# Optimization experiments

Measured on AMD Instinct MI355X. Metric: run time of the kernel, lower is better.

Reference implementation:

```python
import jax, jax.numpy as jnp
import numpy as np

D_MODEL = 512
D_STATE = 16
EXPAND = 2
DT_RANK = 8
D_INNER = EXPAND * D_MODEL  # 1024
LN_EPS = 1e-5


def setup_inputs() -> dict:
    key = jax.random.key(0)
    ks = jax.random.split(key, 10)
    B, H, W = 8, 48, 48
    inp = {
        "x": jax.random.normal(ks[0], (B, H, W, D_MODEL), jnp.float32),
        # Linear weights stored [in, out] (torch weight transposed)
        "W_in": jax.random.normal(ks[1], (D_MODEL, 2 * D_INNER), jnp.float32) * 0.02,
        # depthwise conv kernel, HWIO with feature_group_count = D_INNER
        "conv_k": jax.random.normal(ks[2], (3, 3, 1, D_INNER), jnp.float32) * 0.1,
        "W_xproj": jax.random.normal(ks[3], (D_INNER, DT_RANK + 2 * D_STATE), jnp.float32) * 0.02,
        "W_dt": jax.random.uniform(ks[4], (DT_RANK, D_INNER), jnp.float32, -0.1, 0.1),
        "b_dt": jnp.full((D_INNER,), 0.1, jnp.float32),
        "A_log": jax.random.normal(ks[5], (D_STATE,), jnp.float32) * 0.02,
        "Dskip": jnp.ones((D_INNER,), jnp.float32),
        "W_dtN": jax.random.normal(ks[6], (D_INNER, D_STATE), jnp.float32) * 0.02,
        "b_dtN": jnp.zeros((D_STATE,), jnp.float32),
        "ln_g": jnp.ones((D_INNER,), jnp.float32),
        "ln_b": jnp.zeros((D_INNER,), jnp.float32),
        "W_out": jax.random.normal(ks[7], (D_INNER, D_MODEL), jnp.float32) * 0.02,
        "b_out": jnp.zeros((D_MODEL,), jnp.float32),
    }
    return inp


def _ss2d(x, W_in, conv_k, W_xproj, W_dt, b_dt, A_log, Dskip, W_dtN, b_dtN,
          ln_g, ln_b, W_out, b_out):
    B, H, W_, _ = x.shape
    L = H * W_
    # in_proj and split into x / gate z
    xz = x @ W_in                                   # [B,H,W,2*D_INNER]
    xh, z = jnp.split(xz, 2, axis=-1)
    # depthwise 3x3 conv (NHWC)
    xc = jax.lax.conv_general_dilated(
        xh, conv_k, window_strides=(1, 1), padding='SAME',
        dimension_numbers=('NHWC', 'HWIO', 'NHWC'),
        feature_group_count=D_INNER)                 # [B,H,W,D_INNER]
    # x_proj -> (dt_rank, B, C)
    xp = xc @ W_xproj
    dt_r = xp[..., :DT_RANK]
    Bp = xp[..., DT_RANK:DT_RANK + D_STATE]
    Cp = xp[..., DT_RANK + D_STATE:]
    dt = dt_r @ W_dt + b_dt                          # [B,H,W,D_INNER]
    # flatten spatial dims into sequence
    x_seq = xc.reshape(B, L, D_INNER)
    dt_seq = jax.nn.softplus(dt.reshape(B, L, D_INNER))
    B_seq = Bp.reshape(B, L, D_STATE)
    C_seq = Cp.reshape(B, L, D_STATE)
    A = -jnp.exp(A_log)                              # [N]; A_log expanded over D is constant per-row
    dtN = dt_seq @ W_dtN + b_dtN                     # dt_to_N_proj(softplus(dt)) -> [B,L,N]

    def step(h, t):
        x_t, dt_t, dtN_t, B_t, C_t = t               # [B,D],[B,D],[B,N],[B,N],[B,N]
        dA = jnp.exp(dt_t[:, :, None] * A)           # [B,D,N]
        dB = dtN_t * B_t                             # [B,N]
        h = dA * h + dB[:, None, :] * x_t[:, :, None]  # [B,D,N]
        y = jnp.einsum('bdn,bn->bd', h, C_t) + Dskip * x_t
        return h, y

    h0 = jnp.zeros((B, D_INNER, D_STATE), x.dtype)
    xs = (x_seq.transpose(1, 0, 2), dt_seq.transpose(1, 0, 2),
          dtN.transpose(1, 0, 2), B_seq.transpose(1, 0, 2),
          C_seq.transpose(1, 0, 2))
    _, ys = jax.lax.scan(step, h0, xs)               # ys: [L,B,D]
    y = ys.transpose(1, 0, 2).reshape(B, H, W_, D_INNER)
    # LayerNorm over channel dim
    mu = y.mean(-1, keepdims=True)
    var = ((y - mu) ** 2).mean(-1, keepdims=True)
    y = (y - mu) / jnp.sqrt(var + LN_EPS) * ln_g + ln_b
    # gate and out projection (dropout = identity in eval)
    y = y * jax.nn.silu(z)
    return y @ W_out + b_out


def reference(x, W_in, conv_k, W_xproj, W_dt, b_dt, A_log, Dskip, W_dtN,
              b_dtN, ln_g, ln_b, W_out, b_out):
    return _ss2d(x, W_in, conv_k, W_xproj, W_dt, b_dt, A_log, Dskip, W_dtN,
                 b_dtN, ln_g, ln_b, W_out, b_out)
```

## Files before the change

### kernel.cpp

```cpp
#include <hip/hip_runtime.h>
#include <hip/hip_bf16.h>

#define NBATCH 8
#define HEIGHT 48
#define WIDTH  48
#define DMODEL 512
#define DSTATE 16
#define DTRANK 8
#define DINNER 1024
#define LSEQ   (HEIGHT*WIDTH)
#define NROWS  (NBATCH*LSEQ)
#define NXP    40
#define NCH    64
#define TCH    36

typedef unsigned short u16;
typedef unsigned int   u32;
typedef __attribute__((ext_vector_type(8))) short short8;
typedef __attribute__((ext_vector_type(4))) float f32x4;

__device__ __forceinline__ float bf2f(u16 u) {
    u32 x = ((u32)u) << 16;
    return __uint_as_float(x);
}
__device__ __forceinline__ u16 f2bf(float f) {
    u32 x = __float_as_uint(f);
    u32 r = (x + 0x7FFFu + ((x >> 16) & 1u)) >> 16;
    return (u16)r;
}

#if __has_builtin(__builtin_amdgcn_exp2f)
__device__ __forceinline__ float EXP2(float x) { return __builtin_amdgcn_exp2f(x); }
#else
__device__ __forceinline__ float EXP2(float x) { return __expf(x * 0.69314718f); }
#endif

#define GLD16(g, l) __builtin_amdgcn_global_load_lds( \
    (const __attribute__((address_space(1))) void*)(g), \
    (__attribute__((address_space(3))) void*)(l), 16, 0, 0)

__global__ __launch_bounds__(256) void k_prep_x(const float* __restrict__ x,
                                                u16* __restrict__ xbf) {
    int i = blockIdx.x * 256 + threadIdx.x;
    float4 v = *reinterpret_cast<const float4*>(x + (size_t)i * 4);
    ushort4 o;
    o.x = f2bf(v.x); o.y = f2bf(v.y); o.z = f2bf(v.z); o.w = f2bf(v.w);
    *reinterpret_cast<ushort4*>(xbf + (size_t)i * 4) = o;
}

__global__ __launch_bounds__(256) void k_prep_w(const float* __restrict__ W_in,
                                                const float* __restrict__ W_out,
                                                const float* __restrict__ W_xproj,
                                                const float* __restrict__ W_dtN,
                                                u16* __restrict__ WinT,
                                                u16* __restrict__ WoutT,
                                                u16* __restrict__ WxpB,
                                                u16* __restrict__ WdtNB) {
    int idx = blockIdx.x * 256 + threadIdx.x;
    if (idx < 2048 * 512) {
        int n = idx >> 9, k = idx & 511;
        WinT[idx] = f2bf(W_in[(size_t)k * 2048 + n]);
    } else if (idx < 2048 * 512 + 512 * 1024) {
        int j = idx - 2048 * 512;
        int n = j >> 10, k = j & 1023;
        WoutT[j] = f2bf(W_out[(size_t)k * 512 + n]);
    } else if (idx < 2048 * 512 + 512 * 1024 + 48 * 1024) {
        int j = idx - (2048 * 512 + 512 * 1024);
        int n = j >> 10, k = j & 1023;
        WxpB[j] = (n < NXP) ? f2bf(W_xproj[(size_t)k * NXP + n]) : (u16)0;
    } else {
        int j = idx - (2048 * 512 + 512 * 1024 + 48 * 1024);
        int n = j >> 10, k = j & 1023;
        WdtNB[j] = f2bf(W_dtN[(size_t)k * DSTATE + n]);
    }
}

template<int K, int LDA, int LDB, int LDC, bool F32OUT>
__global__ __launch_bounds__(256) void k_gemm_mfma(const u16* __restrict__ A,
                                                   const u16* __restrict__ B,
                                                   const float* __restrict__ bias,
                                                   void* __restrict__ Cv) {
    __shared__ u16 As[128 * 32];
    __shared__ u16 Bs[128 * 32];
    const int tid = threadIdx.x;
    const int l   = tid & 63;
    const int w   = tid >> 6;
    const int wm  = w >> 1, wn = w & 1;
    const int id   = blockIdx.y * gridDim.x + blockIdx.x;
    const int nwg  = gridDim.x * gridDim.y;
    const int swz  = (id & 7) * (nwg >> 3) + (id >> 3);
    const int bx   = swz % gridDim.x;
    const int by   = swz / gridDim.x;
    const int m0  = by * 128, n0 = bx * 128;
    const int srow = w * 32 + (l >> 2);
    const int sc   = l & 3;
    const int kh = l >> 4;
    const int lr = l & 15;

    f32x4 acc[4][4];
#pragma unroll
    for (int i = 0; i < 4; ++i)
#pragma unroll
        for (int j = 0; j < 4; ++j)
            acc[i][j] = (f32x4){0.f, 0.f, 0.f, 0.f};

    for (int k0 = 0; k0 < K; k0 += 32) {
#pragma unroll
        for (int i = 0; i < 2; ++i) {
            int r  = srow + i * 16;
            int cg = sc ^ ((r >> 1) & 3);
            const u16* ga = A + (size_t)(m0 + r) * LDA + k0 + cg * 8;
            const u16* gb = B + (size_t)(n0 + r) * LDB + k0 + cg * 8;
            GLD16(ga, As + (w * 2 + i) * 512);
            GLD16(gb, Bs + (w * 2 + i) * 512);
        }
        __syncthreads();
        short8 af[4], bfr[4];
#pragma unroll
        for (int f = 0; f < 4; ++f) {
            int ar = wm * 64 + f * 16 + lr;
            af[f]  = *reinterpret_cast<const short8*>(As + ar * 32 + ((kh ^ ((ar >> 1) & 3)) * 8));
            int br = wn * 64 + f * 16 + lr;
            bfr[f] = *reinterpret_cast<const short8*>(Bs + br * 32 + ((kh ^ ((br >> 1) & 3)) * 8));
        }
#pragma unroll
        for (int fm = 0; fm < 4; ++fm)
#pragma unroll
            for (int fn = 0; fn < 4; ++fn)
                acc[fm][fn] = __builtin_amdgcn_mfma_f32_16x16x32_bf16(
                    af[fm], bfr[fn], acc[fm][fn], 0, 0, 0);
        __syncthreads();
    }

#pragma unroll
    for (int fm = 0; fm < 4; ++fm) {
#pragma unroll
        for (int r = 0; r < 4; ++r) {
            int row = m0 + wm * 64 + fm * 16 + (l >> 4) * 4 + r;
#pragma unroll
            for (int fn = 0; fn < 4; ++fn) {
                int col = n0 + wn * 64 + fn * 16 + lr;
                if (F32OUT) {
                    ((float*)Cv)[(size_t)row * LDC + col] = acc[fm][fn][r] + bias[col];
                } else {
                    ((u16*)Cv)[(size_t)row * LDC + col] = f2bf(acc[fm][fn][r]);
                }
            }
        }
    }
}

__global__ __launch_bounds__(256) void k_conv(const u16* __restrict__ xz,
                                              const float* __restrict__ ck,
                                              u16* __restrict__ xc) {
    const int blk = blockIdx.x;
    const int wg = blk % (WIDTH / 8);
    const int hb = blk / (WIDTH / 8);
    const int h = hb % HEIGHT;
    const int b = hb / HEIGHT;
    const int w0 = wg * 8;
    const int c0 = threadIdx.x * 4;

    float acc[8][4];
#pragma unroll
    for (int j = 0; j < 8; ++j)
#pragma unroll
        for (int q = 0; q < 4; ++q) acc[j][q] = 0.f;

#pragma unroll
    for (int kh = 0; kh < 3; ++kh) {
        int hh = h + kh - 1;
        if (hh < 0 || hh >= HEIGHT) continue;
        const u16* rp = xz + ((size_t)(b * HEIGHT + hh) * WIDTH) * 2048 + c0;
        float a[10][4];
#pragma unroll
        for (int i = 0; i < 10; ++i) {
            int ww = w0 - 1 + i;
            if (ww >= 0 && ww < WIDTH) {
                ushort4 v = *reinterpret_cast<const ushort4*>(rp + (size_t)ww * 2048);
                a[i][0] = bf2f(v.x); a[i][1] = bf2f(v.y);
                a[i][2] = bf2f(v.z); a[i][3] = bf2f(v.w);
            } else {
                a[i][0] = a[i][1] = a[i][2] = a[i][3] = 0.f;
            }
        }
#pragma unroll
        for (int kw = 0; kw < 3; ++kw) {
            float4 kv = *reinterpret_cast<const float4*>(ck + (kh * 3 + kw) * DINNER + c0);
#pragma unroll
            for (int j = 0; j < 8; ++j) {
                acc[j][0] = fmaf(a[j + kw][0], kv.x, acc[j][0]);
                acc[j][1] = fmaf(a[j + kw][1], kv.y, acc[j][1]);
                acc[j][2] = fmaf(a[j + kw][2], kv.z, acc[j][2]);
                acc[j][3] = fmaf(a[j + kw][3], kv.w, acc[j][3]);
            }
        }
    }
    const size_t orow = (size_t)((b * HEIGHT + h) * WIDTH + w0);
#pragma unroll
    for (int j = 0; j < 8; ++j) {
        ushort4 ov;
        ov.x = f2bf(acc[j][0]); ov.y = f2bf(acc[j][1]);
        ov.z = f2bf(acc[j][2]); ov.w = f2bf(acc[j][3]);
        *reinterpret_cast<ushort4*>(xc + (orow + j) * DINNER + c0) = ov;
    }
}

__global__ __launch_bounds__(256) void k_xproj(const u16* __restrict__ xc,
                                               const u16* __restrict__ WxpB,
                                               float* __restrict__ xp_out) {
    __shared__ u16 As[64 * 32];
    __shared__ u16 Bs[48 * 32];
    const int tid = threadIdx.x;
    const int l = tid & 63;
    const int w = tid >> 6;
    const int m0 = blockIdx.x * 64;
    const int kh = l >> 4, lr = l & 15;
    const int srow = w * 16 + (l >> 2);
    const int sc = l & 3;

    f32x4 acc[3];
    acc[0] = acc[1] = acc[2] = (f32x4){0.f, 0.f, 0.f, 0.f};

    for (int k0 = 0; k0 < 1024; k0 += 32) {
        {
            int cg = sc ^ ((srow >> 1) & 3);
            GLD16(xc + (size_t)(m0 + srow) * DINNER + k0 + cg * 8, As + w * 512);
            if (w < 3)
                GLD16(WxpB + (size_t)srow * 1024 + k0 + cg * 8, Bs + w * 512);
        }
        __syncthreads();
        int ar = w * 16 + lr;
        short8 af = *reinterpret_cast<const short8*>(As + ar * 32 + ((kh ^ ((ar >> 1) & 3)) * 8));
#pragma unroll
        for (int fn = 0; fn < 3; ++fn) {
            int br = fn * 16 + lr;
            short8 bf = *reinterpret_cast<const short8*>(Bs + br * 32 + ((kh ^ ((br >> 1) & 3)) * 8));
            acc[fn] = __builtin_amdgcn_mfma_f32_16x16x32_bf16(af, bf, acc[fn], 0, 0, 0);
        }
        __syncthreads();
    }
#pragma unroll
    for (int fn = 0; fn < 3; ++fn)
#pragma unroll
        for (int r = 0; r < 4; ++r) {
            int row = m0 + w * 16 + (l >> 4) * 4 + r;
            int col = fn * 16 + lr;
            if (col < NXP) xp_out[(size_t)row * NXP + col] = acc[fn][r];
        }
}

__global__ __launch_bounds__(256) void k_dt(const float* __restrict__ xp,
                                            const float* __restrict__ W_dt,
                                            const float* __restrict__ b_dt,
                                            u16* __restrict__ dt_out) {
    int gid = blockIdx.x * 256 + threadIdx.x;
    int row = gid >> 7;
    int dj  = (gid & 127) * 8;
    const float* xr = xp + (size_t)row * NXP;
    float4 xa = *reinterpret_cast<const float4*>(xr);
    float4 xb = *reinterpret_cast<const float4*>(xr + 4);
    float xv[8] = {xa.x, xa.y, xa.z, xa.w, xb.x, xb.y, xb.z, xb.w};
    float a[8];
    {
        float4 b0 = *reinterpret_cast<const float4*>(b_dt + dj);
        float4 b1 = *reinterpret_cast<const float4*>(b_dt + dj + 4);
        a[0]=b0.x; a[1]=b0.y; a[2]=b0.z; a[3]=b0.w;
        a[4]=b1.x; a[5]=b1.y; a[6]=b1.z; a[7]=b1.w;
    }
#pragma unroll
    for (int j = 0; j < 8; ++j) {
        float4 w0 = *reinterpret_cast<const float4*>(W_dt + j * DINNER + dj);
        float4 w1 = *reinterpret_cast<const float4*>(W_dt + j * DINNER + dj + 4);
        a[0] = fmaf(xv[j], w0.x, a[0]); a[1] = fmaf(xv[j], w0.y, a[1]);
        a[2] = fmaf(xv[j], w0.z, a[2]); a[3] = fmaf(xv[j], w0.w, a[3]);
        a[4] = fmaf(xv[j], w1.x, a[4]); a[5] = fmaf(xv[j], w1.y, a[5]);
        a[6] = fmaf(xv[j], w1.z, a[6]); a[7] = fmaf(xv[j], w1.w, a[7]);
    }
    short8 o;
#pragma unroll
    for (int j = 0; j < 8; ++j) {
        float dt = fmaxf(a[j], 0.f) + log1pf(__expf(-fabsf(a[j])));
        o[j] = (short)f2bf(dt);
    }
    *reinterpret_cast<short8*>(dt_out + (size_t)row * DINNER + dj) = o;
}

__global__ __launch_bounds__(256) void k_dtn(const u16* __restrict__ dtb,
                                             const u16* __restrict__ WdtNB,
                                             const float* __restrict__ b_dtN,
                                             const float* __restrict__ xp,
                                             float* __restrict__ dnBC) {
    __shared__ u16 As[64 * 32];
    __shared__ u16 Bs[16 * 32];
    const int tid = threadIdx.x;
    const int l = tid & 63;
    const int w = tid >> 6;
    const int m0 = blockIdx.x * 64;
    const int kh = l >> 4, lr = l & 15;
    const int srow = w * 16 + (l >> 2);
    const int sc = l & 3;

    f32x4 acc = (f32x4){0.f, 0.f, 0.f, 0.f};

    for (int k0 = 0; k0 < 1024; k0 += 32) {
        {
            int cg = sc ^ ((srow >> 1) & 3);
            GLD16(dtb + (size_t)(m0 + srow) * DINNER + k0 + cg * 8, As + w * 512);
            if (w == 0)
                GLD16(WdtNB + (size_t)srow * 1024 + k0 + cg * 8, Bs);
        }
        __syncthreads();
        int ar = w * 16 + lr;
        short8 af = *reinterpret_cast<const short8*>(As + ar * 32 + ((kh ^ ((ar >> 1) & 3)) * 8));
        short8 bf = *reinterpret_cast<const short8*>(Bs + lr * 32 + ((kh ^ ((lr >> 1) & 3)) * 8));
        acc = __builtin_amdgcn_mfma_f32_16x16x32_bf16(af, bf, acc, 0, 0, 0);
        __syncthreads();
    }
    float bn = b_dtN[lr];
#pragma unroll
    for (int r = 0; r < 4; ++r) {
        int row = m0 + w * 16 + (l >> 4) * 4 + r;
        float dn = acc[r] + bn;
        float Bv = xp[(size_t)row * NXP + DTRANK + lr];
        float Cv = xp[(size_t)row * NXP + DTRANK + DSTATE + lr];
        dnBC[(size_t)row * 32 + lr]      = dn * Bv;
        dnBC[(size_t)row * 32 + 16 + lr] = Cv;
    }
}

#define P1_N(IDX, COMP) \
    dA = EXP2(dt * An2[IDX]); h[IDX] = fmaf(dA, h[IDX], COMP * xt);

#define P1_BODY(T, DTC, XCC, DTN, XCN, PR) { \
    const float4* sv = pS + (size_t)(T) * 8; \
    float4 u0 = sv[0], u1 = sv[1], u2 = sv[2], u3 = sv[3]; \
    if (PR) { DTN = pdt[(size_t)((T) + 1) * DINNER]; \
              XCN = pxc[(size_t)((T) + 1) * DINNER]; } \
    float dt = bf2f(DTC), xt = bf2f(XCC); \
    sdt += dt; \
    float dA; \
    P1_N(0,  u0.x) P1_N(1,  u0.y) P1_N(2,  u0.z) P1_N(3,  u0.w) \
    P1_N(4,  u1.x) P1_N(5,  u1.y) P1_N(6,  u1.z) P1_N(7,  u1.w) \
    P1_N(8,  u2.x) P1_N(9,  u2.y) P1_N(10, u2.z) P1_N(11, u2.w) \
    P1_N(12, u3.x) P1_N(13, u3.y) P1_N(14, u3.z) P1_N(15, u3.w) }

__global__ __launch_bounds__(256) void k_scan_p1(const u16* __restrict__ xc,
                                                 const u16* __restrict__ dtb,
                                                 const float* __restrict__ dnBC,
                                                 const float* __restrict__ A_log,
                                                 float* __restrict__ sdt_out,
                                                 float* __restrict__ Qbuf) {
    const int tid = threadIdx.x;
    const int id  = blockIdx.x;
    const int swz = (id & 7) * ((NBATCH * NCH * 4) >> 3) + (id >> 3);
    const int quarter = swz & 3;
    const int bc = swz >> 2;
    const int c = bc & (NCH - 1);
    const int b = bc >> 6;
    const int d = quarter * 256 + tid;

    float An2[16];
#pragma unroll
    for (int n = 0; n < 16; ++n)
        An2[n] = -__expf(A_log[n]) * 1.44269504f;

    float h[16];
#pragma unroll
    for (int n = 0; n < 16; ++n) h[n] = 0.f;
    float sdt = 0.f;

    const size_t row0 = (size_t)b * LSEQ + (size_t)c * TCH;
    const u16* pdt = dtb + row0 * DINNER + d;
    const u16* pxc = xc  + row0 * DINNER + d;
    const float4* pS = reinterpret_cast<const float4*>(dnBC + row0 * 32);

    u16 dtA = pdt[0], xcA = pxc[0];
    u16 dtB, xcB;

    for (int t = 0; t < TCH - 2; t += 2) {
        P1_BODY(t,     dtA, xcA, dtB, xcB, true)
        P1_BODY(t + 1, dtB, xcB, dtA, xcA, true)
    }
    P1_BODY(TCH - 2, dtA, xcA, dtB, xcB, true)
    P1_BODY(TCH - 1, dtB, xcB, dtA, xcA, false)

    sdt_out[(size_t)bc * DINNER + d] = sdt;
    size_t base = ((size_t)bc << 14) + d;
#pragma unroll
    for (int n = 0; n < 16; ++n)
        Qbuf[base + (size_t)n * DINNER] = h[n];
}

__global__ __launch_bounds__(256) void k_scan_p2(const float* __restrict__ sdt,
                                                 const float* __restrict__ A_log,
                                                 float* __restrict__ Qbuf) {
    int tid = blockIdx.x * 256 + threadIdx.x;
    int b = tid >> 14, rem = tid & 16383;
    int n = rem >> 10, d = rem & 1023;
    float An2 = -__expf(A_log[n]) * 1.44269504f;
    float h = 0.f;
    for (int c = 0; c < NCH; ++c) {
        int bc = b * NCH + c;
        float P = EXP2(sdt[(size_t)bc * DINNER + d] * An2);
        size_t idx = ((size_t)bc << 14) + rem;
        float q = Qbuf[idx];
        Qbuf[idx] = h;
        h = fmaf(P, h, q);
    }
}

#define P3_N(IDX, UC, CC, YS) \
    dA = EXP2(dt * An2[IDX]); h[IDX] = fmaf(dA, h[IDX], UC * xt); \
    YS = fmaf(h[IDX], CC, YS);

#define P3_BODY(T, DTC, XCC, DTN, XCN, PR) { \
    const float4* sv = pS + (size_t)(T) * 8; \
    float4 u0 = sv[0], u1 = sv[1], u2 = sv[2], u3 = sv[3]; \
    float4 c4 = sv[4], c5 = sv[5], c6 = sv[6], c7 = sv[7]; \
    if (PR) { DTN = pdt[(size_t)((T) + 1) * DINNER]; \
              XCN = pxc[(size_t)((T) + 1) * DINNER]; } \
    float dt = bf2f(DTC), xt = bf2f(XCC); \
    float ys0 = Dsk * xt, ys1 = 0.f, ys2 = 0.f, ys3 = 0.f; \
    float dA; \
    P3_N(0,  u0.x, c4.x, ys0) P3_N(1,  u0.y, c4.y, ys1) \
    P3_N(2,  u0.z, c4.z, ys2) P3_N(3,  u0.w, c4.w, ys3) \
    P3_N(4,  u1.x, c5.x, ys0) P3_N(5,  u1.y, c5.y, ys1) \
    P3_N(6,  u1.z, c5.z, ys2) P3_N(7,  u1.w, c5.w, ys3) \
    P3_N(8,  u2.x, c6.x, ys0) P3_N(9,  u2.y, c6.y, ys1) \
    P3_N(10, u2.z, c6.z, ys2) P3_N(11, u2.w, c6.w, ys3) \
    P3_N(12, u3.x, c7.x, ys0) P3_N(13, u3.y, c7.y, ys1) \
    P3_N(14, u3.z, c7.z, ys2) P3_N(15, u3.w, c7.w, ys3) \
    ybuf[(row0 + (T)) * 2048 + d] = f2bf((ys0 + ys1) + (ys2 + ys3)); }

__global__ __launch_bounds__(256) void k_scan_p3(const u16* __restrict__ xc,
                                                 const u16* __restrict__ dtb,
                                                 const float* __restrict__ dnBC,
                                                 const float* __restrict__ A_log,
                                                 const float* __restrict__ Dskip,
                                                 const float* __restrict__ Qbuf,
                                                 u16* __restrict__ ybuf) {
    const int tid = threadIdx.x;
    const int id  = blockIdx.x;
    const int swz = (id & 7) * ((NBATCH * NCH * 4) >> 3) + (id >> 3);
    const int quarter = swz & 3;
    const int bc = swz >> 2;
    const int c = bc & (NCH - 1);
    const int b = bc >> 6;
    const int d = quarter * 256 + tid;

    float An2[16];
#pragma unroll
    for (int n = 0; n < 16; ++n)
        An2[n] = -__expf(A_log[n]) * 1.44269504f;

    float h[16];
    size_t base = ((size_t)bc << 14) + d;
#pragma unroll
    for (int n = 0; n < 16; ++n) h[n] = Qbuf[base + (size_t)n * DINNER];
    float Dsk = Dskip[d];

    const size_t row0 = (size_t)b * LSEQ + (size_t)c * TCH;
    const u16* pdt = dtb + row0 * DINNER + d;
    const u16* pxc = xc  + row0 * DINNER + d;
    const float4* pS = reinterpret_cast<const float4*>(dnBC + row0 * 32);

    u16 dtA = pdt[0], xcA = pxc[0];
    u16 dtB, xcB;

    for (int t = 0; t < TCH - 2; t += 2) {
        P3_BODY(t,     dtA, xcA, dtB, xcB, true)
        P3_BODY(t + 1, dtB, xcB, dtA, xcA, true)
    }
    P3_BODY(TCH - 2, dtA, xcA, dtB, xcB, true)
    P3_BODY(TCH - 1, dtB, xcB, dtA, xcA, false)
}

__global__ __launch_bounds__(256) void k_ln_gate(u16* __restrict__ xz,
                                                 const float* __restrict__ ln_g,
                                                 const float* __restrict__ ln_b) {
    __shared__ float red[8];
    int row = blockIdx.x, tid = threadIdx.x;
    u16* yrow = xz + (size_t)row * 2048;
    int c0 = tid * 4;
    ushort4 v = *reinterpret_cast<const ushort4*>(yrow + c0);
    float y0 = bf2f(v.x), y1 = bf2f(v.y), y2 = bf2f(v.z), y3 = bf2f(v.w);
    float s = y0 + y1 + y2 + y3;
    float q = y0 * y0 + y1 * y1 + y2 * y2 + y3 * y3;
#pragma unroll
    for (int m = 32; m; m >>= 1) {
        s += __shfl_xor(s, m, 64);
        q += __shfl_xor(q, m, 64);
    }
    int lane = tid & 63, wv = tid >> 6;
    if (lane == 0) { red[wv] = s; red[4 + wv] = q; }
    __syncthreads();
    s = red[0] + red[1] + red[2] + red[3];
    q = red[4] + red[5] + red[6] + red[7];
    float mu = s * (1.f / DINNER);
    float var = q * (1.f / DINNER) - mu * mu;
    float rstd = rsqrtf(var + 1e-5f);
    ushort4 zv = *reinterpret_cast<const ushort4*>(yrow + DINNER + c0);
    float4 lg = *reinterpret_cast<const float4*>(ln_g + c0);
    float4 lb = *reinterpret_cast<const float4*>(ln_b + c0);
    float z0 = bf2f(zv.x), z1 = bf2f(zv.y), z2 = bf2f(zv.z), z3 = bf2f(zv.w);
    float g0 = ((y0 - mu) * rstd * lg.x + lb.x) * (z0 / (1.f + __expf(-z0)));
    float g1 = ((y1 - mu) * rstd * lg.y + lb.y) * (z1 / (1.f + __expf(-z1)));
    float g2 = ((y2 - mu) * rstd * lg.z + lb.z) * (z2 / (1.f + __expf(-z2)));
    float g3 = ((y3 - mu) * rstd * lg.w + lb.w) * (z3 / (1.f + __expf(-z3)));
    ushort4 ov;
    ov.x = f2bf(g0); ov.y = f2bf(g1); ov.z = f2bf(g2); ov.w = f2bf(g3);
    *reinterpret_cast<ushort4*>(yrow + c0) = ov;
}

extern "C" void kernel_launch(void* const* d_in, const int* in_sizes, int n_in,
                              void* d_out, int out_size, void* d_ws, size_t ws_size,
                              hipStream_t stream) {
    const float* x       = (const float*)d_in[0];
    const float* W_in    = (const float*)d_in[1];
    const float* conv_k  = (const float*)d_in[2];
    const float* W_xproj = (const float*)d_in[3];
    const float* W_dt    = (const float*)d_in[4];
    const float* b_dt    = (const float*)d_in[5];
    const float* A_log   = (const float*)d_in[6];
    const float* Dskip   = (const float*)d_in[7];
    const float* W_dtN   = (const float*)d_in[8];
    const float* b_dtN   = (const float*)d_in[9];
    const float* ln_g    = (const float*)d_in[10];
    const float* ln_b    = (const float*)d_in[11];
    const float* W_out   = (const float*)d_in[12];
    const float* b_out   = (const float*)d_in[13];
    float* out = (float*)d_out;

    char* ws = (char*)d_ws;
    size_t off = 0;
    u16*   xz    = (u16*)(ws + off); off += (size_t)NROWS * 2048 * 2;
    u16*   xc    = (u16*)(ws + off); off += (size_t)NROWS * 1024 * 2;
    u16*   dtb   = (u16*)(ws + off); off += (size_t)NROWS * 1024 * 2;
    float* xpb   = (float*)(ws + off); off += (size_t)NROWS * NXP * 4;
    float* dnBC  = (float*)(ws + off); off += (size_t)NROWS * 32 * 4;
    char*  scr   = ws + off; off += (size_t)NBATCH * NCH * DINNER * DSTATE * 4;
    u16*   xbf   = (u16*)scr;
    float* Qbuf  = (float*)scr;
    float* sdtb  = xpb;
    u16*   WinT  = (u16*)(ws + off); off += (size_t)2048 * 512 * 2;
    u16*   WoutT = (u16*)(ws + off); off += (size_t)512 * 1024 * 2;
    u16*   WxpB  = (u16*)(ws + off); off += (size_t)48 * 1024 * 2;
    u16*   WdtNB = (u16*)(ws + off); off += (size_t)16 * 1024 * 2;

    k_prep_x<<<(NROWS * DMODEL / 4) / 256, 256, 0, stream>>>(x, xbf);
    k_prep_w<<<(2048 * 512 + 512 * 1024 + 48 * 1024 + 16 * 1024) / 256, 256, 0, stream>>>(
        W_in, W_out, W_xproj, W_dtN, WinT, WoutT, WxpB, WdtNB);
    k_gemm_mfma<512, 512, 512, 2048, false>
        <<<dim3(2048 / 128, NROWS / 128), 256, 0, stream>>>(xbf, WinT, nullptr, xz);
    k_conv<<<NBATCH * HEIGHT * (WIDTH / 8), 256, 0, stream>>>(xz, conv_k, xc);
    k_xproj<<<NROWS / 64, 256, 0, stream>>>(xc, WxpB, xpb);
    k_dt<<<(NROWS * DINNER / 8) / 256, 256, 0, stream>>>(xpb, W_dt, b_dt, dtb);
    k_dtn<<<NROWS / 64, 256, 0, stream>>>(dtb, WdtNB, b_dtN, xpb, dnBC);
    k_scan_p1<<<NBATCH * NCH * 4, 256, 0, stream>>>(xc, dtb, dnBC, A_log,
                                                    sdtb, Qbuf);
    k_scan_p2<<<(NBATCH * DINNER * DSTATE) / 256, 256, 0, stream>>>(sdtb, A_log, Qbuf);
    k_scan_p3<<<NBATCH * NCH * 4, 256, 0, stream>>>(xc, dtb, dnBC, A_log,
                                                    Dskip, Qbuf, xz);
    k_ln_gate<<<NROWS, 256, 0, stream>>>(xz, ln_g, ln_b);
    k_gemm_mfma<1024, 2048, 1024, 512, true>
        <<<dim3(DMODEL / 128, NROWS / 128), 256, 0, stream>>>(xz, WoutT, b_out, out);
}
```

Before: 330.9 us.

## Fuse x_proj with dt projection, split-K skinny GEMMs, merge prep kernels

Merges the x and weight bf16 prep kernels into one launch, and fuses the x_proj GEMM with the dt low-rank projection plus softplus so xp does not need a round trip for dt. The skinny x_proj and dt_N GEMMs are restructured as 16-row tiles with split-K across four waves, reading operands straight from global memory and reducing through LDS instead of staging through LDS with barriers. It also raises wave priority around the scan inner math. The aim is fewer launches, more blocks for these narrow GEMMs and less barrier overhead. The cost is an extra LDS reduction and redundant W_dt loads per block.

```diff
diff --git a/kernel.cpp b/kernel.cpp
--- a/kernel.cpp
+++ b/kernel.cpp
@@ -39,24 +39,25 @@
     (const __attribute__((address_space(1))) void*)(g), \
     (__attribute__((address_space(3))) void*)(l), 16, 0, 0)
 
-__global__ __launch_bounds__(256) void k_prep_x(const float* __restrict__ x,
-                                                u16* __restrict__ xbf) {
-    int i = blockIdx.x * 256 + threadIdx.x;
-    float4 v = *reinterpret_cast<const float4*>(x + (size_t)i * 4);
-    ushort4 o;
-    o.x = f2bf(v.x); o.y = f2bf(v.y); o.z = f2bf(v.z); o.w = f2bf(v.w);
-    *reinterpret_cast<ushort4*>(xbf + (size_t)i * 4) = o;
-}
-
-__global__ __launch_bounds__(256) void k_prep_w(const float* __restrict__ W_in,
-                                                const float* __restrict__ W_out,
-                                                const float* __restrict__ W_xproj,
-                                                const float* __restrict__ W_dtN,
-                                                u16* __restrict__ WinT,
-                                                u16* __restrict__ WoutT,
-                                                u16* __restrict__ WxpB,
-                                                u16* __restrict__ WdtNB) {
-    int idx = blockIdx.x * 256 + threadIdx.x;
+__global__ __launch_bounds__(256) void k_prep(const float* __restrict__ x,
+                                              const float* __restrict__ W_in,
+                                              const float* __restrict__ W_out,
+                                              const float* __restrict__ W_xproj,
+                                              const float* __restrict__ W_dtN,
+                                              u16* __restrict__ xbf,
+                                              u16* __restrict__ WinT,
+                                              u16* __restrict__ WoutT,
+                                              u16* __restrict__ WxpB,
+                                              u16* __restrict__ WdtNB) {
+    if (blockIdx.x < 9216) {
+        int i = blockIdx.x * 256 + threadIdx.x;
+        float4 v = *reinterpret_cast<const float4*>(x + (size_t)i * 4);
+        ushort4 o;
+        o.x = f2bf(v.x); o.y = f2bf(v.y); o.z = f2bf(v.z); o.w = f2bf(v.w);
+        *reinterpret_cast<ushort4*>(xbf + (size_t)i * 4) = o;
+        return;
+    }
+    int idx = (blockIdx.x - 9216) * 256 + threadIdx.x;
     if (idx < 2048 * 512) {
         int n = idx >> 9, k = idx & 511;
         WinT[idx] = f2bf(W_in[(size_t)k * 2048 + n]);
@@ -206,84 +207,71 @@
     }
 }
 
-__global__ __launch_bounds__(256) void k_xproj(const u16* __restrict__ xc,
-                                               const u16* __restrict__ WxpB,
-                                               float* __restrict__ xp_out) {
-    __shared__ u16 As[64 * 32];
-    __shared__ u16 Bs[48 * 32];
+__global__ __launch_bounds__(256) void k_xproj_dt(const u16* __restrict__ xc,
+                                                  const u16* __restrict__ WxpB,
+                                                  const float* __restrict__ W_dt,
+                                                  const float* __restrict__ b_dt,
+                                                  float* __restrict__ xp_out,
+                                                  u16* __restrict__ dt_out) {
+    __shared__ float R[4][16][48];
+    __shared__ float xpS[16][8];
     const int tid = threadIdx.x;
-    const int l = tid & 63;
-    const int w = tid >> 6;
-    const int m0 = blockIdx.x * 64;
-    const int kh = l >> 4, lr = l & 15;
-    const int srow = w * 16 + (l >> 2);
-    const int sc = l & 3;
+    const int l = tid & 63, w = tid >> 6;
+    const int m0 = blockIdx.x * 16;
+    const int lr = l & 15, kh = l >> 4;
+    const int kbase = w * 256;
 
     f32x4 acc[3];
     acc[0] = acc[1] = acc[2] = (f32x4){0.f, 0.f, 0.f, 0.f};
-
-    for (int k0 = 0; k0 < 1024; k0 += 32) {
-        {
-            int cg = sc ^ ((srow >> 1) & 3);
-            GLD16(xc + (size_t)(m0 + srow) * DINNER + k0 + cg * 8, As + w * 512);
-            if (w < 3)
-                GLD16(WxpB + (size_t)srow * 1024 + k0 + cg * 8, Bs + w * 512);
-        }
-        __syncthreads();
-        int ar = w * 16 + lr;
-        short8 af = *reinterpret_cast<const short8*>(As + ar * 32 + ((kh ^ ((ar >> 1) & 3)) * 8));
+    const u16* arow = xc + (size_t)(m0 + lr) * DINNER + kbase + kh * 8;
+#pragma unroll
+    for (int ks = 0; ks < 256; ks += 32) {
+        short8 af = *reinterpret_cast<const short8*>(arow + ks);
 #pragma unroll
         for (int fn = 0; fn < 3; ++fn) {
-            int br = fn * 16 + lr;
-            short8 bf = *reinterpret_cast<const short8*>(Bs + br * 32 + ((kh ^ ((br >> 1) & 3)) * 8));
+            short8 bf = *reinterpret_cast<const short8*>(
+                WxpB + (size_t)(fn * 16 + lr) * DINNER + kbase + ks + kh * 8);
             acc[fn] = __builtin_amdgcn_mfma_f32_16x16x32_bf16(af, bf, acc[fn], 0, 0, 0);
         }
-        __syncthreads();
     }
 #pragma unroll
     for (int fn = 0; fn < 3; ++fn)
 #pragma unroll
-        for (int r = 0; r < 4; ++r) {
-            int row = m0 + w * 16 + (l >> 4) * 4 + r;
-            int col = fn * 16 + lr;
-            if (col < NXP) xp_out[(size_t)row * NXP + col] = acc[fn][r];
-        }
-}
-
-__global__ __launch_bounds__(256) void k_dt(const float* __restrict__ xp,
-                                            const float* __restrict__ W_dt,
-                                            const float* __restrict__ b_dt,
-                                            u16* __restrict__ dt_out) {
-    int gid = blockIdx.x * 256 + threadIdx.x;
-    int row = gid >> 7;
-    int dj  = (gid & 127) * 8;
-    const float* xr = xp + (size_t)row * NXP;
-    float4 xa = *reinterpret_cast<const float4*>(xr);
-    float4 xb = *reinterpret_cast<const float4*>(xr + 4);
-    float xv[8] = {xa.x, xa.y, xa.z, xa.w, xb.x, xb.y, xb.z, xb.w};
-    float a[8];
-    {
-        float4 b0 = *reinterpret_cast<const float4*>(b_dt + dj);
-        float4 b1 = *reinterpret_cast<const float4*>(b_dt + dj + 4);
-        a[0]=b0.x; a[1]=b0.y; a[2]=b0.z; a[3]=b0.w;
-        a[4]=b1.x; a[5]=b1.y; a[6]=b1.z; a[7]=b1.w;
-    }
+        for (int r = 0; r < 4; ++r)
+            R[w][(l >> 4) * 4 + r][fn * 16 + lr] = acc[fn][r];
+    __syncthreads();
+    for (int i = tid; i < 16 * 48; i += 256) {
+        int row = i / 48, col = i % 48;
+        float s = R[0][row][col] + R[1][row][col] + R[2][row][col] + R[3][row][col];
+        if (col < NXP) xp_out[(size_t)(m0 + row) * NXP + col] = s;
+        if (col < 8) xpS[row][col] = s;
+    }
+    __syncthreads();
+    const int d4 = tid * 4;
+    float wreg[8][4];
 #pragma unroll
     for (int j = 0; j < 8; ++j) {
-        float4 w0 = *reinterpret_cast<const float4*>(W_dt + j * DINNER + dj);
-        float4 w1 = *reinterpret_cast<const float4*>(W_dt + j * DINNER + dj + 4);
-        a[0] = fmaf(xv[j], w0.x, a[0]); a[1] = fmaf(xv[j], w0.y, a[1]);
-        a[2] = fmaf(xv[j], w0.z, a[2]); a[3] = fmaf(xv[j], w0.w, a[3]);
-        a[4] = fmaf(xv[j], w1.x, a[4]); a[5] = fmaf(xv[j], w1.y, a[5]);
-        a[6] = fmaf(xv[j], w1.z, a[6]); a[7] = fmaf(xv[j], w1.w, a[7]);
-    }
-    short8 o;
-#pragma unroll
-    for (int j = 0; j < 8; ++j) {
-        float dt = fmaxf(a[j], 0.f) + log1pf(__expf(-fabsf(a[j])));
-        o[j] = (short)f2bf(dt);
-    }
-    *reinterpret_cast<short8*>(dt_out + (size_t)row * DINNER + dj) = o;
+        float4 wv = *reinterpret_cast<const float4*>(W_dt + j * DINNER + d4);
+        wreg[j][0] = wv.x; wreg[j][1] = wv.y; wreg[j][2] = wv.z; wreg[j][3] = wv.w;
+    }
+    float4 bb = *reinterpret_cast<const float4*>(b_dt + d4);
+    for (int row = 0; row < 16; ++row) {
+        float a0 = bb.x, a1 = bb.y, a2 = bb.z, a3 = bb.w;
+#pragma unroll
+        for (int j = 0; j < 8; ++j) {
+            float xj = xpS[row][j];
+            a0 = fmaf(xj, wreg[j][0], a0);
+            a1 = fmaf(xj, wreg[j][1], a1);
+            a2 = fmaf(xj, wreg[j][2], a2);
+            a3 = fmaf(xj, wreg[j][3], a3);
+        }
+        ushort4 o;
+        o.x = f2bf(fmaxf(a0, 0.f) + log1pf(__expf(-fabsf(a0))));
+        o.y = f2bf(fmaxf(a1, 0.f) + log1pf(__expf(-fabsf(a1))));
+        o.z = f2bf(fmaxf(a2, 0.f) + log1pf(__expf(-fabsf(a2))));
+        o.w = f2bf(fmaxf(a3, 0.f) + log1pf(__expf(-fabsf(a3))));
+        *reinterpret_cast<ushort4*>(dt_out + (size_t)(m0 + row) * DINNER + d4) = o;
+    }
 }
 
 __global__ __launch_bounds__(256) void k_dtn(const u16* __restrict__ dtb,
@@ -291,42 +279,32 @@
                                              const float* __restrict__ b_dtN,
                                              const float* __restrict__ xp,
                                              float* __restrict__ dnBC) {
-    __shared__ u16 As[64 * 32];
-    __shared__ u16 Bs[16 * 32];
+    __shared__ float R[4][16][16];
     const int tid = threadIdx.x;
-    const int l = tid & 63;
-    const int w = tid >> 6;
-    const int m0 = blockIdx.x * 64;
-    const int kh = l >> 4, lr = l & 15;
-    const int srow = w * 16 + (l >> 2);
-    const int sc = l & 3;
+    const int l = tid & 63, w = tid >> 6;
+    const int m0 = blockIdx.x * 16;
+    const int lr = l & 15, kh = l >> 4;
+    const int kbase = w * 256;
 
     f32x4 acc = (f32x4){0.f, 0.f, 0.f, 0.f};
-
-    for (int k0 = 0; k0 < 1024; k0 += 32) {
-        {
-            int cg = sc ^ ((srow >> 1) & 3);
-            GLD16(dtb + (size_t)(m0 + srow) * DINNER + k0 + cg * 8, As + w * 512);
-            if (w == 0)
-                GLD16(WdtNB + (size_t)srow * 1024 + k0 + cg * 8, Bs);
-        }
-        __syncthreads();
-        int ar = w * 16 + lr;
-        short8 af = *reinterpret_cast<const short8*>(As + ar * 32 + ((kh ^ ((ar >> 1) & 3)) * 8));
-        short8 bf = *reinterpret_cast<const short8*>(Bs + lr * 32 + ((kh ^ ((lr >> 1) & 3)) * 8));
+    const u16* arow = dtb + (size_t)(m0 + lr) * DINNER + kbase + kh * 8;
+    const u16* brow = WdtNB + (size_t)lr * DINNER + kbase + kh * 8;
+#pragma unroll
+    for (int ks = 0; ks < 256; ks += 32) {
+        short8 af = *reinterpret_cast<const short8*>(arow + ks);
+        short8 bf = *reinterpret_cast<const short8*>(brow + ks);
         acc = __builtin_amdgcn_mfma_f32_16x16x32_bf16(af, bf, acc, 0, 0, 0);
-        __syncthreads();
-    }
-    float bn = b_dtN[lr];
-#pragma unroll
-    for (int r = 0; r < 4; ++r) {
-        int row = m0 + w * 16 + (l >> 4) * 4 + r;
-        float dn = acc[r] + bn;
-        float Bv = xp[(size_t)row * NXP + DTRANK + lr];
-        float Cv = xp[(size_t)row * NXP + DTRANK + DSTATE + lr];
-        dnBC[(size_t)row * 32 + lr]      = dn * Bv;
-        dnBC[(size_t)row * 32 + 16 + lr] = Cv;
-    }
+    }
+#pragma unroll
+    for (int r = 0; r < 4; ++r)
+        R[w][(l >> 4) * 4 + r][lr] = acc[r];
+    __syncthreads();
+    int row = tid >> 4, n = tid & 15;
+    float dn = R[0][row][n] + R[1][row][n] + R[2][row][n] + R[3][row][n] + b_dtN[n];
+    float Bv = xp[(size_t)(m0 + row) * NXP + DTRANK + n];
+    float Cv = xp[(size_t)(m0 + row) * NXP + DTRANK + DSTATE + n];
+    dnBC[(size_t)(m0 + row) * 32 + n]      = dn * Bv;
+    dnBC[(size_t)(m0 + row) * 32 + 16 + n] = Cv;
 }
 
 #define P1_N(IDX, COMP) \
@@ -340,10 +318,12 @@
     float dt = bf2f(DTC), xt = bf2f(XCC); \
     sdt += dt; \
     float dA; \
+    __builtin_amdgcn_s_setprio(1); \
     P1_N(0,  u0.x) P1_N(1,  u0.y) P1_N(2,  u0.z) P1_N(3,  u0.w) \
     P1_N(4,  u1.x) P1_N(5,  u1.y) P1_N(6,  u1.z) P1_N(7,  u1.w) \
     P1_N(8,  u2.x) P1_N(9,  u2.y) P1_N(10, u2.z) P1_N(11, u2.w) \
-    P1_N(12, u3.x) P1_N(13, u3.y) P1_N(14, u3.z) P1_N(15, u3.w) }
+    P1_N(12, u3.x) P1_N(13, u3.y) P1_N(14, u3.z) P1_N(15, u3.w) \
+    __builtin_amdgcn_s_setprio(0); }
 
 __global__ __launch_bounds__(256) void k_scan_p1(const u16* __restrict__ xc,
                                                  const u16* __restrict__ dtb,
@@ -423,6 +403,7 @@
     float dt = bf2f(DTC), xt = bf2f(XCC); \
     float ys0 = Dsk * xt, ys1 = 0.f, ys2 = 0.f, ys3 = 0.f; \
     float dA; \
+    __builtin_amdgcn_s_setprio(1); \
     P3_N(0,  u0.x, c4.x, ys0) P3_N(1,  u0.y, c4.y, ys1) \
     P3_N(2,  u0.z, c4.z, ys2) P3_N(3,  u0.w, c4.w, ys3) \
     P3_N(4,  u1.x, c5.x, ys0) P3_N(5,  u1.y, c5.y, ys1) \
@@ -431,6 +412,7 @@
     P3_N(10, u2.z, c6.z, ys2) P3_N(11, u2.w, c6.w, ys3) \
     P3_N(12, u3.x, c7.x, ys0) P3_N(13, u3.y, c7.y, ys1) \
     P3_N(14, u3.z, c7.z, ys2) P3_N(15, u3.w, c7.w, ys3) \
+    __builtin_amdgcn_s_setprio(0); \
     ybuf[(row0 + (T)) * 2048 + d] = f2bf((ys0 + ys1) + (ys2 + ys3)); }
 
 __global__ __launch_bounds__(256) void k_scan_p3(const u16* __restrict__ xc,
@@ -548,15 +530,13 @@
     u16*   WxpB  = (u16*)(ws + off); off += (size_t)48 * 1024 * 2;
     u16*   WdtNB = (u16*)(ws + off); off += (size_t)16 * 1024 * 2;
 
-    k_prep_x<<<(NROWS * DMODEL / 4) / 256, 256, 0, stream>>>(x, xbf);
-    k_prep_w<<<(2048 * 512 + 512 * 1024 + 48 * 1024 + 16 * 1024) / 256, 256, 0, stream>>>(
-        W_in, W_out, W_xproj, W_dtN, WinT, WoutT, WxpB, WdtNB);
+    k_prep<<<9216 + 6400, 256, 0, stream>>>(x, W_in, W_out, W_xproj, W_dtN,
+                                            xbf, WinT, WoutT, WxpB, WdtNB);
     k_gemm_mfma<512, 512, 512, 2048, false>
         <<<dim3(2048 / 128, NROWS / 128), 256, 0, stream>>>(xbf, WinT, nullptr, xz);
     k_conv<<<NBATCH * HEIGHT * (WIDTH / 8), 256, 0, stream>>>(xz, conv_k, xc);
-    k_xproj<<<NROWS / 64, 256, 0, stream>>>(xc, WxpB, xpb);
-    k_dt<<<(NROWS * DINNER / 8) / 256, 256, 0, stream>>>(xpb, W_dt, b_dt, dtb);
-    k_dtn<<<NROWS / 64, 256, 0, stream>>>(dtb, WdtNB, b_dtN, xpb, dnBC);
+    k_xproj_dt<<<NROWS / 16, 256, 0, stream>>>(xc, WxpB, W_dt, b_dt, xpb, dtb);
+    k_dtn<<<NROWS / 16, 256, 0, stream>>>(dtb, WdtNB, b_dtN, xpb, dnBC);
     k_scan_p1<<<NBATCH * NCH * 4, 256, 0, stream>>>(xc, dtb, dnBC, A_log,
                                                     sdtb, Qbuf);
     k_scan_p2<<<(NBATCH * DINNER * DSTATE) / 256, 256, 0, stream>>>(sdtb, A_log, Qbuf);
```

Result: slower. 340.3 us (+2.8%).
